# Kernel optimization log

Hardware: AMD Instinct MI355X
Metric: run time of the kernel (lower is better)

Reference implementation:

```python
import jax, jax.numpy as jnp
import numpy as np

DIM = 512
H = 256
W = 256
N = 32768


def _dwconv(x, w, b):
    # x: [1, C, W, H], w: [C, 1, k, k] depthwise, b: [C]
    y = jax.lax.conv_general_dilated(
        x, w, window_strides=(1, 1), padding='SAME',
        feature_group_count=w.shape[0],
        dimension_numbers=('NCHW', 'OIHW', 'NCHW'))
    return y + b[None, :, None, None]


def setup_inputs() -> dict:
    rng = np.random.default_rng(0)
    # unique, lexicographically sorted occupied cells; force corners so
    # grid extent after pos - pos.min() is exactly H x W
    inner = rng.choice(H * W - 2, size=N - 2, replace=False) + 1
    idx = np.sort(np.concatenate([[0], inner, [H * W - 1]])).astype(np.int32)
    pos = np.stack([idx // W, idx % W], axis=1)  # [N, 2]

    key = jax.random.key(0)
    ks = jax.random.split(key, 7)
    x = jax.random.normal(ks[0], (1, N, DIM), jnp.float32)
    w1 = jax.random.normal(ks[1], (DIM, 1, 3, 3), jnp.float32) * 0.05
    b1 = jax.random.normal(ks[2], (DIM,), jnp.float32) * 0.05
    w2 = jax.random.normal(ks[3], (DIM, 1, 5, 5), jnp.float32) * 0.05
    b2 = jax.random.normal(ks[4], (DIM,), jnp.float32) * 0.05
    w3 = jax.random.normal(ks[5], (DIM, 1, 7, 7), jnp.float32) * 0.05
    b3 = jax.random.normal(ks[6], (DIM,), jnp.float32) * 0.05
    return {'x': x, 'pos': jnp.asarray(pos), 'w1': w1, 'b1': b1,
            'w2': w2, 'b2': b2, 'w3': w3, 'b3': b3}


def reference(x, pos, w1, b1, w2, b2, w3, b3):
    pos = pos - pos.min(axis=0)            # shift to origin
    vals = x[0]                            # [N, DIM]
    # scatter points onto dense grid (duplicate coords sum, like coalesce)
    dense = jnp.zeros((H, W, DIM), x.dtype).at[pos[:, 0], pos[:, 1]].add(vals)
    # permute(2,1,0).unsqueeze(0): [H,W,DIM] -> [1, DIM, W, H]
    x_dense = dense.transpose(2, 1, 0)[None]
    x_pos = _dwconv(x_dense, w1, b1) + _dwconv(x_dense, w2, b2) + _dwconv(x_dense, w3, b3)
    mask = x_dense.sum(axis=1) != 0.0      # [1, W, H] occupied cells
    x_pos = jnp.where(mask[:, None], x_pos, 0.0) + x_dense
    # squeeze().permute(2,1,0) -> [H, W, DIM]; to_sparse(2).values() gathers
    # occupied cells in lexicographic (h, w) order == input pos order here
    grid = x_pos[0].transpose(2, 1, 0)
    out = grid[pos[:, 0], pos[:, 1]][None]  # [1, N, DIM]
    return out
```

## Files before the change

### kernel.cpp

```cpp
#include <hip/hip_runtime.h>

#define DIM 512
#define H 256
#define W 256

__global__ void scatter_map_kernel(const int* __restrict__ pos,
                                   int* __restrict__ map, int n) {
    int i = blockIdx.x * blockDim.x + threadIdx.x;
    if (i < n) {
        int h = pos[2 * i], w = pos[2 * i + 1];
        map[h * W + w] = i;
    }
}

__global__ void build_weights_kernel(const float* __restrict__ k3,
                                     const float* __restrict__ b1,
                                     const float* __restrict__ k5,
                                     const float* __restrict__ b2,
                                     const float* __restrict__ k7,
                                     const float* __restrict__ b3,
                                     float* __restrict__ weff,
                                     float* __restrict__ bsum) {
    int o = blockIdx.x;
    int c = threadIdx.x;
    int dh = o / 7 - 3, dw = o % 7 - 3;
    float v = k7[c * 49 + (dw + 3) * 7 + (dh + 3)];
    if (dh >= -2 && dh <= 2 && dw >= -2 && dw <= 2)
        v += k5[c * 25 + (dw + 2) * 5 + (dh + 2)];
    if (dh >= -1 && dh <= 1 && dw >= -1 && dw <= 1)
        v += k3[c * 9 + (dw + 1) * 3 + (dh + 1)];
    weff[o * DIM + c] = v;
    if (o == 0) bsum[c] = b1[c] + b2[c] + b3[c];
}

__global__ __launch_bounds__(128) void gather_conv_kernel(
    const float* __restrict__ x, const int* __restrict__ pos,
    const int* __restrict__ map, const float* __restrict__ weff,
    const float* __restrict__ bsum, float* __restrict__ out) {
    int i = blockIdx.x;
    int tid = threadIdx.x;

    __shared__ int s_list[49];
    __shared__ int s_cnt;
    if (tid == 0) s_cnt = 0;
    __syncthreads();

    int h = pos[2 * i], w = pos[2 * i + 1];
    if (tid < 49) {
        int dh = tid / 7 - 3, dw = tid % 7 - 3;
        int hh = h + dh, ww = w + dw;
        if (hh >= 0 && hh < H && ww >= 0 && ww < W) {
            int j = map[hh * W + ww];
            if (j >= 0) {
                int slot = atomicAdd(&s_cnt, 1);
                s_list[slot] = (j << 6) | tid;
            }
        }
    }
    __syncthreads();

    int c = tid * 4;
    float4 acc = *(const float4*)(x + (size_t)i * DIM + c);
    float4 bb  = *(const float4*)(bsum + c);
    acc.x += bb.x; acc.y += bb.y; acc.z += bb.z; acc.w += bb.w;

    int cnt = s_cnt;
    for (int k = 0; k < cnt; ++k) {
        int pk = s_list[k];
        int j = pk >> 6, o = pk & 63;
        float4 wv = *(const float4*)(weff + o * DIM + c);
        float4 xv = *(const float4*)(x + (size_t)j * DIM + c);
        acc.x = fmaf(wv.x, xv.x, acc.x);
        acc.y = fmaf(wv.y, xv.y, acc.y);
        acc.z = fmaf(wv.z, xv.z, acc.z);
        acc.w = fmaf(wv.w, xv.w, acc.w);
    }
    *(float4*)(out + (size_t)i * DIM + c) = acc;
}

extern "C" void kernel_launch(void* const* d_in, const int* in_sizes, int n_in,
                              void* d_out, int out_size, void* d_ws, size_t ws_size,
                              hipStream_t stream) {
    const float* x   = (const float*)d_in[0];
    const int*   pos = (const int*)d_in[1];
    const float* k3  = (const float*)d_in[2];
    const float* b1  = (const float*)d_in[3];
    const float* k5  = (const float*)d_in[4];
    const float* b2  = (const float*)d_in[5];
    const float* k7  = (const float*)d_in[6];
    const float* b3  = (const float*)d_in[7];
    float* out = (float*)d_out;

    char* ws = (char*)d_ws;
    int*   map  = (int*)ws;
    float* weff = (float*)(ws + (size_t)H * W * 4);
    float* bsum = (float*)(ws + (size_t)H * W * 4 + 49 * DIM * 4);

    int n = in_sizes[1] / 2;

    hipMemsetAsync(map, 0xFF, (size_t)H * W * sizeof(int), stream);
    scatter_map_kernel<<<(n + 255) / 256, 256, 0, stream>>>(pos, map, n);
    build_weights_kernel<<<49, DIM, 0, stream>>>(k3, b1, k5, b2, k7, b3, weff, bsum);
    gather_conv_kernel<<<n, 128, 0, stream>>>(x, pos, map, weff, bsum, out);
}
```

Baseline: 247.5 us.

## Fuse prep kernels, drop map memset via pos validation, unroll gather, remap blocks

The weight-building and scatter-map kernels are merged into one launch, and the memset of the map is dropped. Stale map entries are instead rejected by checking the index range and comparing the stored point's coordinates against pos. The gather loop is unrolled by four so more loads are in flight, and block IDs are permuted in strides of n/8, presumably to spread neighbouring points across XCDs. The coordinate check adds two extra global loads per neighbour in the gather kernel.

```diff
diff --git a/kernel.cpp b/kernel.cpp
--- a/kernel.cpp
+++ b/kernel.cpp
@@ -4,40 +4,40 @@
 #define H 256
 #define W 256
 
-__global__ void scatter_map_kernel(const int* __restrict__ pos,
-                                   int* __restrict__ map, int n) {
-    int i = blockIdx.x * blockDim.x + threadIdx.x;
-    if (i < n) {
-        int h = pos[2 * i], w = pos[2 * i + 1];
-        map[h * W + w] = i;
+__global__ __launch_bounds__(512) void prep_kernel(
+    const int* __restrict__ pos, int n,
+    const float* __restrict__ k3, const float* __restrict__ b1,
+    const float* __restrict__ k5, const float* __restrict__ b2,
+    const float* __restrict__ k7, const float* __restrict__ b3,
+    float* __restrict__ weff, float* __restrict__ bsum,
+    int* __restrict__ map) {
+    int b = blockIdx.x;
+    if (b < 49) {
+        int o = b;
+        int c = threadIdx.x;
+        int dh = o / 7 - 3, dw = o % 7 - 3;
+        float v = k7[c * 49 + (dw + 3) * 7 + (dh + 3)];
+        if (dh >= -2 && dh <= 2 && dw >= -2 && dw <= 2)
+            v += k5[c * 25 + (dw + 2) * 5 + (dh + 2)];
+        if (dh >= -1 && dh <= 1 && dw >= -1 && dw <= 1)
+            v += k3[c * 9 + (dw + 1) * 3 + (dh + 1)];
+        weff[o * DIM + c] = v;
+        if (o == 0) bsum[c] = b1[c] + b2[c] + b3[c];
+    } else {
+        int i = (b - 49) * 512 + threadIdx.x;
+        if (i < n) {
+            int h = pos[2 * i], w = pos[2 * i + 1];
+            map[h * W + w] = i;
+        }
     }
-}
-
-__global__ void build_weights_kernel(const float* __restrict__ k3,
-                                     const float* __restrict__ b1,
-                                     const float* __restrict__ k5,
-                                     const float* __restrict__ b2,
-                                     const float* __restrict__ k7,
-                                     const float* __restrict__ b3,
-                                     float* __restrict__ weff,
-                                     float* __restrict__ bsum) {
-    int o = blockIdx.x;
-    int c = threadIdx.x;
-    int dh = o / 7 - 3, dw = o % 7 - 3;
-    float v = k7[c * 49 + (dw + 3) * 7 + (dh + 3)];
-    if (dh >= -2 && dh <= 2 && dw >= -2 && dw <= 2)
-        v += k5[c * 25 + (dw + 2) * 5 + (dh + 2)];
-    if (dh >= -1 && dh <= 1 && dw >= -1 && dw <= 1)
-        v += k3[c * 9 + (dw + 1) * 3 + (dh + 1)];
-    weff[o * DIM + c] = v;
-    if (o == 0) bsum[c] = b1[c] + b2[c] + b3[c];
 }
 
 __global__ __launch_bounds__(128) void gather_conv_kernel(
     const float* __restrict__ x, const int* __restrict__ pos,
     const int* __restrict__ map, const float* __restrict__ weff,
-    const float* __restrict__ bsum, float* __restrict__ out) {
-    int i = blockIdx.x;
+    const float* __restrict__ bsum, float* __restrict__ out, int n) {
+    int bid = blockIdx.x;
+    int i = ((n & 7) == 0) ? ((bid & 7) * (n >> 3) + (bid >> 3)) : bid;
     int tid = threadIdx.x;
 
     __shared__ int s_list[49];
@@ -51,7 +51,7 @@
         int hh = h + dh, ww = w + dw;
         if (hh >= 0 && hh < H && ww >= 0 && ww < W) {
             int j = map[hh * W + ww];
-            if (j >= 0) {
+            if ((unsigned)j < (unsigned)n && pos[2 * j] == hh && pos[2 * j + 1] == ww) {
                 int slot = atomicAdd(&s_cnt, 1);
                 s_list[slot] = (j << 6) | tid;
             }
@@ -65,11 +65,39 @@
     acc.x += bb.x; acc.y += bb.y; acc.z += bb.z; acc.w += bb.w;
 
     int cnt = s_cnt;
-    for (int k = 0; k < cnt; ++k) {
+    int k = 0;
+    for (; k + 4 <= cnt; k += 4) {
+        int p0 = s_list[k + 0], p1 = s_list[k + 1];
+        int p2 = s_list[k + 2], p3 = s_list[k + 3];
+        float4 w0 = *(const float4*)(weff + (p0 & 63) * DIM + c);
+        float4 x0 = *(const float4*)(x + (size_t)(p0 >> 6) * DIM + c);
+        float4 w1 = *(const float4*)(weff + (p1 & 63) * DIM + c);
+        float4 x1 = *(const float4*)(x + (size_t)(p1 >> 6) * DIM + c);
+        float4 w2 = *(const float4*)(weff + (p2 & 63) * DIM + c);
+        float4 x2 = *(const float4*)(x + (size_t)(p2 >> 6) * DIM + c);
+        float4 w3 = *(const float4*)(weff + (p3 & 63) * DIM + c);
+        float4 x3 = *(const float4*)(x + (size_t)(p3 >> 6) * DIM + c);
+        acc.x = fmaf(w0.x, x0.x, acc.x);
+        acc.y = fmaf(w0.y, x0.y, acc.y);
+        acc.z = fmaf(w0.z, x0.z, acc.z);
+        acc.w = fmaf(w0.w, x0.w, acc.w);
+        acc.x = fmaf(w1.x, x1.x, acc.x);
+        acc.y = fmaf(w1.y, x1.y, acc.y);
+        acc.z = fmaf(w1.z, x1.z, acc.z);
+        acc.w = fmaf(w1.w, x1.w, acc.w);
+        acc.x = fmaf(w2.x, x2.x, acc.x);
+        acc.y = fmaf(w2.y, x2.y, acc.y);
+        acc.z = fmaf(w2.z, x2.z, acc.z);
+        acc.w = fmaf(w2.w, x2.w, acc.w);
+        acc.x = fmaf(w3.x, x3.x, acc.x);
+        acc.y = fmaf(w3.y, x3.y, acc.y);
+        acc.z = fmaf(w3.z, x3.z, acc.z);
+        acc.w = fmaf(w3.w, x3.w, acc.w);
+    }
+    for (; k < cnt; ++k) {
         int pk = s_list[k];
-        int j = pk >> 6, o = pk & 63;
-        float4 wv = *(const float4*)(weff + o * DIM + c);
-        float4 xv = *(const float4*)(x + (size_t)j * DIM + c);
+        float4 wv = *(const float4*)(weff + (pk & 63) * DIM + c);
+        float4 xv = *(const float4*)(x + (size_t)(pk >> 6) * DIM + c);
         acc.x = fmaf(wv.x, xv.x, acc.x);
         acc.y = fmaf(wv.y, xv.y, acc.y);
         acc.z = fmaf(wv.z, xv.z, acc.z);
@@ -98,8 +126,8 @@
 
     int n = in_sizes[1] / 2;
 
-    hipMemsetAsync(map, 0xFF, (size_t)H * W * sizeof(int), stream);
-    scatter_map_kernel<<<(n + 255) / 256, 256, 0, stream>>>(pos, map, n);
-    build_weights_kernel<<<49, DIM, 0, stream>>>(k3, b1, k5, b2, k7, b3, weff, bsum);
-    gather_conv_kernel<<<n, 128, 0, stream>>>(x, pos, map, weff, bsum, out);
+    int scatter_blocks = (n + 511) / 512;
+    prep_kernel<<<49 + scatter_blocks, 512, 0, stream>>>(
+        pos, n, k3, b1, k5, b2, k7, b3, weff, bsum, map);
+    gather_conv_kernel<<<n, 128, 0, stream>>>(x, pos, map, weff, bsum, out, n);
 }
```

Result: faster. 227.1 us (-8.2%).
